# Kernel tuning notes

Hardware: AMD Instinct MI355X
Metric: run time of the kernel (lower is better)

## Reference

```python
import jax, jax.numpy as jnp
import numpy as np

N = 100_000      # number of sparse voxels / points
M = 1_000_000    # number of kernel-map (key,query) pairs
C_IN = 128
C_OUT = 128
H = 8            # num_heads
CH = C_OUT // H  # attn_channels = 16
KVOL = 27        # kernel_volume for kernel_size=3, dim=3
EPS_BN = 1e-5
EPS_NORM = 1e-12


def _bn(x, gamma, beta):
    # BatchNorm1d in training mode: batch statistics over point dim
    mu = jnp.mean(x, axis=0)
    var = jnp.var(x, axis=0)
    return (x - mu) * jax.lax.rsqrt(var + EPS_BN) * gamma + beta


def _l2norm(x):
    # F.normalize(p=2, dim=-1) with eps clamp
    n = jnp.sqrt(jnp.sum(x * x, axis=-1, keepdims=True))
    return x / jnp.maximum(n, EPS_NORM)


def setup_inputs() -> dict:
    key = jax.random.key(0)
    ks = jax.random.split(key, 14)
    inp = {
        "points": jax.random.normal(ks[0], (N, 3), jnp.float32),
        "feats": jax.random.normal(ks[1], (N, C_IN), jnp.float32),
        "k_idx": jax.random.randint(ks[2], (M,), 0, N),
        "q_idx": jax.random.randint(ks[3], (M,), 0, N),
        "kernel_idx": jax.random.randint(ks[4], (M,), 0, KVOL),
        # intra_pos_mlp params: Linear(3,3,no bias)-BN-ReLU-Linear(3,C_IN,no bias)-BN-ReLU-Linear(C_IN,C_IN)
        "w1": jax.random.normal(ks[5], (3, 3), jnp.float32) / np.float32(np.sqrt(3.0)),
        "g1": jnp.ones((3,), jnp.float32),
        "b1": jnp.zeros((3,), jnp.float32),
        "w2": jax.random.normal(ks[6], (3, C_IN), jnp.float32) / np.float32(np.sqrt(3.0)),
        "g2": jnp.ones((C_IN,), jnp.float32),
        "b2": jnp.zeros((C_IN,), jnp.float32),
        "w3": jax.random.normal(ks[7], (C_IN, C_IN), jnp.float32) / np.float32(np.sqrt(C_IN)),
        "b3": jnp.zeros((C_IN,), jnp.float32),
        # to_query / to_value (1x1 Minkowski conv == per-point linear) and to_out
        "wq": jax.random.normal(ks[8], (C_IN, C_OUT), jnp.float32) / np.float32(np.sqrt(C_IN)),
        "bq": jnp.zeros((C_OUT,), jnp.float32),
        "wv": jax.random.normal(ks[9], (C_IN, C_OUT), jnp.float32) / np.float32(np.sqrt(C_IN)),
        "bv": jnp.zeros((C_OUT,), jnp.float32),
        "wo": jax.random.normal(ks[10], (C_OUT, C_OUT), jnp.float32) / np.float32(np.sqrt(C_OUT)),
        "bo": jnp.zeros((C_OUT,), jnp.float32),
        # inter_pos_enc ~ N(0,1) per nn.init.normal_
        "pos_enc": jax.random.normal(ks[11], (KVOL, H, CH), jnp.float32),
    }
    return inp


def reference(points, feats, k_idx, q_idx, kernel_idx,
              w1, g1, b1, w2, g2, b2, w3, b3,
              wq, bq, wv, bv, wo, bo, pos_enc):
    # intra positional encoding MLP, added to features
    h = jax.nn.relu(_bn(points @ w1, g1, b1))
    h = jax.nn.relu(_bn(h @ w2, g2, b2))
    x = feats + (h @ w3 + b3)                       # [N, C_IN]
    # per-point query / value projections
    q = (x @ wq + bq).reshape(N, H, CH)             # [N, H, CH]
    v = (x @ wv + bv).reshape(N, H, CH)
    qn = _l2norm(q)
    pn = _l2norm(pos_enc)                           # [KVOL, H, CH]
    # DotProduct op: attn[m,h] = <norm_q[q_idx[m],h], norm_pos_enc[kernel_idx[m],h]>
    attn = jnp.einsum('mhc,mhc->mh', qn[q_idx], pn[kernel_idx])  # [M, H]
    # ScalarAttention op: out[q_idx[m],h,:] += attn[m,h] * v[k_idx[m],h,:]
    out = jnp.zeros((N, H, CH), feats.dtype).at[q_idx].add(attn[:, :, None] * v[k_idx])
    # to_out linear
    return out.reshape(N, C_OUT) @ wo + bo          # [N, C_OUT]
```

## Files before the change

### kernel.cpp

```cpp
#include <hip/hip_runtime.h>
#include <hip/hip_bf16.h>

#define CIN 128
#define NHEAD 8
#define CHD 16
#define KVOL 27
#define NBKT_MAX 512
#define CH 4096
#define NB1 64
#define NB2 256

constexpr float EPS_BN = 1e-5f;
constexpr float EPS_NORM = 1e-12f;

typedef __attribute__((ext_vector_type(8))) short short8;
typedef __attribute__((ext_vector_type(4))) float f32x4;

__device__ __forceinline__ float bflo(unsigned u) {
  return __uint_as_float(u << 16);
}
__device__ __forceinline__ float bfhi(unsigned u) {
  return __uint_as_float(u & 0xffff0000u);
}
__device__ __forceinline__ float bfus(unsigned short u) {
  return __uint_as_float((unsigned)u << 16);
}
__device__ __forceinline__ unsigned pk2bf(float lo, float hi) {
  __hip_bfloat16 a = __float2bfloat16(lo), b = __float2bfloat16(hi);
  return (unsigned)*(unsigned short*)&a | ((unsigned)*(unsigned short*)&b << 16);
}

__global__ __launch_bounds__(256) void k_bn1_stats(
    const float* __restrict__ points, const float* __restrict__ w1,
    float* __restrict__ partials1, int N) {
  __shared__ float red[4][6];
  float w[9];
#pragma unroll
  for (int i = 0; i < 9; ++i) w[i] = w1[i];
  float s[3] = {0.f, 0.f, 0.f}, ss[3] = {0.f, 0.f, 0.f};
  for (int n = blockIdx.x * blockDim.x + threadIdx.x; n < N;
       n += gridDim.x * blockDim.x) {
    float p0 = points[3 * n], p1 = points[3 * n + 1], p2 = points[3 * n + 2];
#pragma unroll
    for (int j = 0; j < 3; ++j) {
      float y = p0 * w[j] + p1 * w[3 + j] + p2 * w[6 + j];
      s[j] += y;
      ss[j] += y * y;
    }
  }
#pragma unroll
  for (int j = 0; j < 3; ++j) {
    for (int off = 32; off > 0; off >>= 1) {
      s[j] += __shfl_down(s[j], off);
      ss[j] += __shfl_down(ss[j], off);
    }
  }
  int t = threadIdx.x;
  if ((t & 63) == 0) {
    int wv = t >> 6;
#pragma unroll
    for (int j = 0; j < 3; ++j) {
      red[wv][j] = s[j];
      red[wv][3 + j] = ss[j];
    }
  }
  __syncthreads();
  if (t < 6) {
    float acc = red[0][t] + red[1][t] + red[2][t] + red[3][t];
    partials1[blockIdx.x * 8 + t] = acc;
  }
}

__global__ __launch_bounds__(256) void k_bn2_stats(
    const float* __restrict__ points, const float* __restrict__ w1,
    const float* __restrict__ g1, const float* __restrict__ b1,
    const float* __restrict__ w2, const float* __restrict__ partials1,
    float* __restrict__ partials2, int N) {
  __shared__ float pa[256][3];
  int t = threadIdx.x;
  float w[9];
#pragma unroll
  for (int i = 0; i < 9; ++i) w[i] = w1[i];
  float st[6] = {0.f, 0.f, 0.f, 0.f, 0.f, 0.f};
  for (int b = 0; b < NB1; ++b)
#pragma unroll
    for (int j = 0; j < 6; ++j) st[j] += partials1[b * 8 + j];
  float sc1[3], sh1[3];
#pragma unroll
  for (int j = 0; j < 3; ++j) {
    float m = st[j] / (float)N;
    float var = st[3 + j] / (float)N - m * m;
    float sc = rsqrtf(var + EPS_BN) * g1[j];
    sc1[j] = sc;
    sh1[j] = b1[j] - m * sc;
  }
  int c = t & 127, half = t >> 7;
  float wc0 = w2[c], wc1 = w2[CIN + c], wc2 = w2[2 * CIN + c];
  float s = 0.f, ss = 0.f;
  for (int base = blockIdx.x * 256; base < N; base += gridDim.x * 256) {
    int np = min(256, N - base);
    __syncthreads();
    if (t < np) {
      int n = base + t;
      float p0 = points[3 * n], p1 = points[3 * n + 1], p2 = points[3 * n + 2];
      float y0 = p0 * w[0] + p1 * w[3] + p2 * w[6];
      float y1 = p0 * w[1] + p1 * w[4] + p2 * w[7];
      float y2 = p0 * w[2] + p1 * w[5] + p2 * w[8];
      pa[t][0] = fmaxf(y0 * sc1[0] + sh1[0], 0.f);
      pa[t][1] = fmaxf(y1 * sc1[1] + sh1[1], 0.f);
      pa[t][2] = fmaxf(y2 * sc1[2] + sh1[2], 0.f);
    }
    __syncthreads();
    for (int p = half; p < np; p += 2) {
      float y = pa[p][0] * wc0 + pa[p][1] * wc1 + pa[p][2] * wc2;
      s += y;
      ss += y * y;
    }
  }
  __syncthreads();
  float* red = (float*)pa;
  red[t] = s;
  red[256 + t] = ss;
  __syncthreads();
  if (t < 128) {
    partials2[blockIdx.x * CIN + t] = red[t] + red[128 + t];
    partials2[NB2 * CIN + blockIdx.x * CIN + t] =
        red[256 + t] + red[256 + 128 + t];
  }
}

__global__ __launch_bounds__(256) void k_red2(const float* __restrict__ partials1,
                                              const float* __restrict__ partials2,
                                              float* __restrict__ stats1,
                                              float* __restrict__ stats2) {
  int t = threadIdx.x;
  if (t < 128) {
    float s = 0.f, ss = 0.f;
    for (int b = 0; b < NB2; ++b) {
      s += partials2[b * CIN + t];
      ss += partials2[NB2 * CIN + b * CIN + t];
    }
    stats2[t] = s;
    stats2[CIN + t] = ss;
  } else if (t < 134) {
    int j = t - 128;
    float s = 0.f;
    for (int b = 0; b < NB1; ++b) s += partials1[b * 8 + j];
    stats1[j] = s;
  }
}

__global__ void k_prep(const float* __restrict__ pos_enc,
                       const float* __restrict__ wq,
                       const float* __restrict__ wv,
                       const float* __restrict__ wo,
                       const float* __restrict__ w3,
                       __hip_bfloat16* __restrict__ pnb,
                       __hip_bfloat16* __restrict__ wqT,
                       __hip_bfloat16* __restrict__ wvT,
                       __hip_bfloat16* __restrict__ woT,
                       __hip_bfloat16* __restrict__ w3b) {
  int g = blockIdx.x * 256 + threadIdx.x;
  if (g < 256) {
    int kk = g >> 3, h = g & 7;
    if (kk < KVOL) {
      const float* src = pos_enc + (kk * NHEAD + h) * CHD;
      float vals[CHD];
      float s = 0.f;
#pragma unroll
      for (int i = 0; i < CHD; ++i) {
        vals[i] = src[i];
        s += vals[i] * vals[i];
      }
      float inv = 1.f / fmaxf(sqrtf(s), EPS_NORM);
#pragma unroll
      for (int i = 0; i < CHD; ++i)
        pnb[kk * CIN + h * CHD + i] = __float2bfloat16(vals[i] * inv);
    } else {
#pragma unroll
      for (int i = 0; i < CHD; ++i)
        pnb[kk * CIN + h * CHD + i] = __float2bfloat16(0.f);
    }
  }
  if (g < CIN * CIN) {
    int k = g >> 7, c = g & 127;
    int gt = c * CIN + k;
    wqT[gt] = __float2bfloat16(wq[g]);
    wvT[gt] = __float2bfloat16(wv[g]);
    woT[gt] = __float2bfloat16(wo[g]);
    w3b[g] = __float2bfloat16(w3[g]);
  }
}

__global__ __launch_bounds__(256) void k_prep2(
    const __hip_bfloat16* __restrict__ w3b,
    const __hip_bfloat16* __restrict__ wqT,
    const __hip_bfloat16* __restrict__ wvT, const float* __restrict__ wq,
    const float* __restrict__ wv, const float* __restrict__ b3,
    const float* __restrict__ bq, const float* __restrict__ bv,
    __hip_bfloat16* __restrict__ W3qT, __hip_bfloat16* __restrict__ W3vT,
    float* __restrict__ bqp, float* __restrict__ bvp) {
  int t = threadIdx.x;
  if (blockIdx.x == 4) {
    int c = t & 127;
    const float* wsel = (t < 128) ? wq : wv;
    float s = (t < 128) ? bq[c] : bv[c];
    for (int j = 0; j < CIN; ++j) s += b3[j] * wsel[j * CIN + c];
    if (t < 128)
      bqp[c] = s;
    else
      bvp[c] = s;
    return;
  }
  int n0 = blockIdx.x * 32;
  int w = t >> 6, l = t & 63;
  int lr = l & 15, lg = l >> 4;
  int colbase = w * 32;
  f32x4 cq[2][2], cv[2][2];
#pragma unroll
  for (int mt = 0; mt < 2; ++mt)
#pragma unroll
    for (int nt = 0; nt < 2; ++nt) {
      cq[mt][nt] = {0.f, 0.f, 0.f, 0.f};
      cv[mt][nt] = {0.f, 0.f, 0.f, 0.f};
    }
#pragma unroll
  for (int kk = 0; kk < 4; ++kk) {
    short8 aA[2], bQ[2], bV[2];
#pragma unroll
    for (int mt = 0; mt < 2; ++mt)
      aA[mt] = *(const short8*)(w3b + (size_t)(n0 + mt * 16 + lr) * CIN +
                                kk * 32 + lg * 8);
#pragma unroll
    for (int nt = 0; nt < 2; ++nt) {
      size_t off = (size_t)(colbase + nt * 16 + lr) * CIN + kk * 32 + lg * 8;
      bQ[nt] = *(const short8*)(wqT + off);
      bV[nt] = *(const short8*)(wvT + off);
    }
#pragma unroll
    for (int mt = 0; mt < 2; ++mt)
#pragma unroll
      for (int nt = 0; nt < 2; ++nt) {
        cq[mt][nt] = __builtin_amdgcn_mfma_f32_16x16x32_bf16(aA[mt], bQ[nt],
                                                             cq[mt][nt], 0, 0, 0);
        cv[mt][nt] = __builtin_amdgcn_mfma_f32_16x16x32_bf16(aA[mt], bV[nt],
                                                             cv[mt][nt], 0, 0, 0);
      }
  }
#pragma unroll
  for (int mt = 0; mt < 2; ++mt)
#pragma unroll
    for (int nt = 0; nt < 2; ++nt)
#pragma unroll
      for (int r = 0; r < 4; ++r) {
        int k = n0 + mt * 16 + lg * 4 + r;
        int c = colbase + nt * 16 + lr;
        W3qT[(size_t)c * CIN + k] = __float2bfloat16(cq[mt][nt][r]);
        W3vT[(size_t)c * CIN + k] = __float2bfloat16(cv[mt][nt][r]);
      }
}

__global__ __launch_bounds__(256) void k_chist(const int* __restrict__ q_idx,
                                               int* __restrict__ ccnt, int M) {
  __shared__ int lh[NBKT_MAX];
  int t = threadIdx.x;
  for (int b = t; b < NBKT_MAX; b += 256) lh[b] = 0;
  __syncthreads();
  for (int i = blockIdx.x * 256 + t; i < M; i += gridDim.x * 256)
    atomicAdd(&lh[q_idx[i] >> 8], 1);
  __syncthreads();
  for (int b = t; b < NBKT_MAX; b += 256) {
    int c = lh[b];
    if (c > 0) atomicAdd(&ccnt[b], c);
  }
}

__global__ __launch_bounds__(256) void k_cscan(const int* __restrict__ ccnt,
                                               int* __restrict__ sbase,
                                               int* __restrict__ bcur) {
  __shared__ int wsum[4];
  int t = threadIdx.x;
  int s0 = ccnt[2 * t], s1 = ccnt[2 * t + 1];
  int s = s0 + s1;
  int l = t & 63, w = t >> 6;
  int ss = s;
  for (int off = 1; off < 64; off <<= 1) {
    int v = __shfl_up(ss, off);
    if (l >= off) ss += v;
  }
  if (l == 63) wsum[w] = ss;
  __syncthreads();
  int wb = 0;
#pragma unroll
  for (int i = 0; i < 4; ++i)
    if (i < w) wb += wsum[i];
  int ex = wb + ss - s;
  sbase[2 * t] = ex;
  sbase[2 * t + 1] = ex + s0;
  bcur[2 * t] = ex;
  bcur[2 * t + 1] = ex + s0;
  if (t == 255) sbase[NBKT_MAX] = wb + ss;
}

__global__ __launch_bounds__(256) void k_bucket1(
    const int* __restrict__ q_idx, const int* __restrict__ k_idx,
    const int* __restrict__ kernel_idx, int* __restrict__ bcur,
    unsigned* __restrict__ stg, int M) {
  __shared__ int lhist[NBKT_MAX];
  __shared__ int loffs[NBKT_MAX];
  __shared__ int lcur[NBKT_MAX];
  __shared__ int wsum[4];
  __shared__ unsigned buf[CH];
  int t = threadIdx.x;
  int base = blockIdx.x * CH;
  for (int b = t; b < NBKT_MAX; b += 256) lhist[b] = 0;
  __syncthreads();

  int qv[16];
#pragma unroll
  for (int j = 0; j < 16; ++j) {
    int i = base + t + j * 256;
    int q = (i < M) ? q_idx[i] : -1;
    qv[j] = q;
    if (q >= 0) atomicAdd(&lhist[q >> 8], 1);
  }
  __syncthreads();

  {
    int s0 = lhist[2 * t], s1 = lhist[2 * t + 1];
    int s = s0 + s1;
    int l = t & 63, w = t >> 6;
    int ss = s;
    for (int off = 1; off < 64; off <<= 1) {
      int v = __shfl_up(ss, off);
      if (l >= off) ss += v;
    }
    if (l == 63) wsum[w] = ss;
    __syncthreads();
    int wb = 0;
#pragma unroll
    for (int i = 0; i < 4; ++i)
      if (i < w) wb += wsum[i];
    int ex = wb + ss - s;
    loffs[2 * t] = ex;
    loffs[2 * t + 1] = ex + s0;
    lcur[2 * t] = ex;
    lcur[2 * t + 1] = ex + s0;
  }
  __syncthreads();

#pragma unroll
  for (int j = 0; j < 16; ++j) {
    int q = qv[j];
    if (q >= 0) {
      int i = base + t + j * 256;
      unsigned e = (unsigned)k_idx[i] | ((unsigned)kernel_idx[i] << 17) |
                   ((unsigned)(q & 255) << 22);
      int d = atomicAdd(&lcur[q >> 8], 1);
      buf[d] = e;
    }
  }
  __syncthreads();

  for (int b = t; b < NBKT_MAX; b += 256) {
    int cntb = lhist[b];
    if (cntb > 0) {
      int g = atomicAdd(&bcur[b], cntb);
      int lo = loffs[b];
      for (int j = 0; j < cntb; ++j) stg[g + j] = buf[lo + j];
    }
  }
}

__global__ __launch_bounds__(256) void k_bucket2a(
    const unsigned* __restrict__ stg, const int* __restrict__ sbase,
    int* __restrict__ cnt, int N) {
  __shared__ int lh[256];
  int b = blockIdx.x;
  int t = threadIdx.x;
  lh[t] = 0;
  __syncthreads();
  int start = sbase[b];
  int bcnt = sbase[b + 1] - start;
  for (int i = t; i < bcnt; i += 256) atomicAdd(&lh[stg[start + i] >> 22], 1);
  __syncthreads();
  int q = (b << 8) + t;
  if (q < N) cnt[q] = lh[t];
}

__global__ __launch_bounds__(256) void k_scan1(const int* __restrict__ cnt,
                                               int* __restrict__ poffs,
                                               int* __restrict__ bsum, int N) {
  __shared__ int ws_[4];
  int t = threadIdx.x;
  int l = t & 63, w = t >> 6;
  int base = blockIdx.x * 1024 + t * 4;
  int pc[4];
  int s = 0;
#pragma unroll
  for (int j = 0; j < 4; ++j) {
    int c = (base + j < N) ? cnt[base + j] : 0;
    pc[j] = (c + 7) & ~7;
// ... 31 lines not shown
    int v = __shfl_up(s, off);
    if (l >= off) s += v;
  }
  if (l == 63) ws_[w] = s;
  __syncthreads();
  int wbase = 0;
#pragma unroll
  for (int i = 0; i < 4; ++i)
    if (i < w) wbase += ws_[i];
  if (t < NB) bbase[t] = wbase + s - own;
  if (t == 255) *poffsN = wbase + s;
}

__global__ __launch_bounds__(256) void k_scan3(const int* __restrict__ cnt,
                                               int* __restrict__ poffs,
                                               const int* __restrict__ bbase,
                                               unsigned* __restrict__ recs,
                                               int N) {
  int t = threadIdx.x;
  int base = blockIdx.x * 1024 + t * 4;
  int bb = bbase[blockIdx.x];
#pragma unroll
  for (int j = 0; j < 4; ++j) {
    int i = base + j;
    if (i >= N) break;
    int o = poffs[i] + bb;
    poffs[i] = o;
    int c = cnt[i];
    int pcend = o + ((c + 7) & ~7);
    for (int p = o + c; p < pcend; ++p) recs[p] = 27u << 17;
  }
}

__global__ __launch_bounds__(256) void k_bucket2b(
    const unsigned* __restrict__ stg, const int* __restrict__ sbase,
    const int* __restrict__ poffs, unsigned* __restrict__ recs, int N) {
  __shared__ int qcur[256];
  int b = blockIdx.x;
  int t = threadIdx.x;
  int qbase = b << 8;
  int q = qbase + t;
  qcur[t] = (q < N) ? poffs[q] : 0;
  __syncthreads();
  int start = sbase[b];
  int bcnt = sbase[b + 1] - start;
  for (int i = t; i < bcnt; i += 256) {
    unsigned e = stg[start + i];
    int ql = e >> 22;
    unsigned rec = e & 0x3FFFFFu;
    int pos = atomicAdd(&qcur[ql], 1);
    recs[pos] = rec;
  }
}

__global__ __launch_bounds__(256) void k_qv(
    const float* __restrict__ points, const float* __restrict__ feats,
    const float* __restrict__ w1, const float* __restrict__ g1,
    const float* __restrict__ b1, const float* __restrict__ w2,
    const float* __restrict__ g2, const float* __restrict__ b2,
    const __hip_bfloat16* __restrict__ wqT,
    const __hip_bfloat16* __restrict__ wvT,
    const __hip_bfloat16* __restrict__ W3qT,
    const __hip_bfloat16* __restrict__ W3vT, const float* __restrict__ bqp,
    const float* __restrict__ bvp, const float* __restrict__ stats1,
    const float* __restrict__ stats2, __hip_bfloat16* __restrict__ qnout,
    __hip_bfloat16* __restrict__ vout, int N) {
  __shared__ float h0s[32][3];
  __shared__ __hip_bfloat16 h1s[32][136];
  __shared__ __hip_bfloat16 fs[32][136];

  int t = threadIdx.x;
  int n0 = blockIdx.x * 32;

  int frow = t >> 3, fpart = t & 7;
  int fn = n0 + frow;
  float4 f0 = {0.f, 0.f, 0.f, 0.f}, f1 = f0, f2 = f0, f3 = f0;
  if (fn < N) {
    const float4* src = (const float4*)(feats + (size_t)fn * CIN + fpart * 16);
    f0 = src[0];
    f1 = src[1];
    f2 = src[2];
    f3 = src[3];
  }

  if (t < 32) {
    int n = n0 + t;
    float p0 = 0.f, p1 = 0.f, p2 = 0.f;
    if (n < N) {
      p0 = points[3 * n];
      p1 = points[3 * n + 1];
      p2 = points[3 * n + 2];
    }
#pragma unroll
    for (int j = 0; j < 3; ++j) {
      float m = stats1[j] / (float)N;
      float var = stats1[3 + j] / (float)N - m * m;
      float sc = rsqrtf(var + EPS_BN) * g1[j];
      float sh = b1[j] - m * sc;
      float y = p0 * w1[j] + p1 * w1[3 + j] + p2 * w1[6 + j];
      h0s[t][j] = fmaxf(y * sc + sh, 0.f);
    }
  }

  {
    unsigned u[8];
// ... 91 lines not shown
        s += __shfl_xor(s, 4);
        s += __shfl_xor(s, 8);
        float inv = 1.f / fmaxf(sqrtf(s), EPS_NORM);
        int row = mt * 16 + lg * 4 + r;
        int col = colbase + nt * 16 + lr;
        fs[row][col] = __float2bfloat16(q * inv);
        h1s[row][col] = __float2bfloat16(av[mt][nt][r]);
      }
  __syncthreads();

  {
    int row = t >> 3, part = t & 7;
    int n = n0 + row;
    if (n < N) {
      const char* srcq = (const char*)&fs[row][0] + part * 32;
      char* dstq = (char*)qnout + (size_t)n * 256 + part * 32;
      *(uint4*)dstq = *(const uint4*)srcq;
      *(uint4*)(dstq + 16) = *(const uint4*)(srcq + 16);
      const char* srcv = (const char*)&h1s[row][0] + part * 32;
      char* dstv = (char*)vout + (size_t)n * 256 + part * 32;
      *(uint4*)dstv = *(const uint4*)srcv;
      *(uint4*)(dstv + 16) = *(const uint4*)(srcv + 16);
    }
  }
}

__global__ __launch_bounds__(512) void k_gather_out(
    const unsigned* __restrict__ recs, const int* __restrict__ poffs,
    const __hip_bfloat16* __restrict__ qn, const __hip_bfloat16* __restrict__ v,
    const __hip_bfloat16* __restrict__ pnb,
    const __hip_bfloat16* __restrict__ woT, const float* __restrict__ bo,
    float* __restrict__ out, int N) {
  __shared__ __hip_bfloat16 accs[32][136];
  __shared__ unsigned short dotlds[32][256];
  int t = threadIdx.x;
  int w = t >> 6, l = t & 63;
  int h = l >> 3;
  int n0 = blockIdx.x * 32;
  const char* vbase = (const char*)v + 4 * l;

  {
    int row = t >> 4, part = t & 15;
    int n = n0 + row;
    uint4 val = {0u, 0u, 0u, 0u};
    if (n < N)
      val = *(const uint4*)((const char*)qn + (size_t)n * 256 + part * 16);
    *(uint4*)((char*)&accs[row][0] + part * 16) = val;
  }
  __syncthreads();

  {
    int lr = l & 15, lg = l >> 4;
    int rg = w & 1;
    const short8 zero8 = {0, 0, 0, 0, 0, 0, 0, 0};
#pragma unroll
    for (int hh = 0; hh < 2; ++hh) {
      int hx = (w >> 1) * 2 + hh;
      short8 aA = zero8, bB0 = zero8, bB1 = zero8;
      if (lg < 2) {
        aA = *(const short8*)((const char*)&accs[rg * 16 + lr][0] +
                              (hx * CHD + lg * 8) * 2);
        bB0 = *(const short8*)(pnb + lr * CIN + hx * CHD + lg * 8);
        bB1 = *(const short8*)(pnb + (16 + lr) * CIN + hx * CHD + lg * 8);
      }
      f32x4 c0 = {0.f, 0.f, 0.f, 0.f}, c1 = {0.f, 0.f, 0.f, 0.f};
      c0 = __builtin_amdgcn_mfma_f32_16x16x32_bf16(aA, bB0, c0, 0, 0, 0);
      c1 = __builtin_amdgcn_mfma_f32_16x16x32_bf16(aA, bB1, c1, 0, 0, 0);
#pragma unroll
      for (int r = 0; r < 4; ++r) {
        int row = rg * 16 + lg * 4 + r;
        __hip_bfloat16 b0 = __float2bfloat16(c0[r]);
        __hip_bfloat16 b1 = __float2bfloat16(c1[r]);
        dotlds[row][lr * 8 + hx] = *(unsigned short*)&b0;
        dotlds[row][(16 + lr) * 8 + hx] = *(unsigned short*)&b1;
      }
    }
  }
  __syncthreads();

#pragma unroll 1
  for (int j = 0; j < 4; ++j) {
    int nl = w * 4 + j;
    int n = n0 + nl;
    float ax = 0.f, ay = 0.f;
    if (n < N) {
      const unsigned short* dptr = &dotlds[nl][0];
      int beg = poffs[n], end = poffs[n + 1];
      for (int idx = beg; idx < end; idx += 8) {
        unsigned r0 = recs[idx + 0], r1 = recs[idx + 1], r2 = recs[idx + 2],
                 r3 = recs[idx + 3], r4 = recs[idx + 4], r5 = recs[idx + 5],
                 r6 = recs[idx + 6], r7 = recs[idx + 7];
        unsigned v0 = *(const unsigned*)(vbase + (size_t)(r0 & 0x1FFFF) * 256);
        unsigned v1 = *(const unsigned*)(vbase + (size_t)(r1 & 0x1FFFF) * 256);
        unsigned v2 = *(const unsigned*)(vbase + (size_t)(r2 & 0x1FFFF) * 256);
        unsigned v3 = *(const unsigned*)(vbase + (size_t)(r3 & 0x1FFFF) * 256);
        unsigned v4 = *(const unsigned*)(vbase + (size_t)(r4 & 0x1FFFF) * 256);
        unsigned v5 = *(const unsigned*)(vbase + (size_t)(r5 & 0x1FFFF) * 256);
        unsigned v6 = *(const unsigned*)(vbase + (size_t)(r6 & 0x1FFFF) * 256);
        unsigned v7 = *(const unsigned*)(vbase + (size_t)(r7 & 0x1FFFF) * 256);
        float a0 = bfus(dptr[(r0 >> 17) * 8 + h]);
        float a1 = bfus(dptr[(r1 >> 17) * 8 + h]);
        float a2 = bfus(dptr[(r2 >> 17) * 8 + h]);
        float a3 = bfus(dptr[(r3 >> 17) * 8 + h]);
        float a4 = bfus(dptr[(r4 >> 17) * 8 + h]);
        float a5 = bfus(dptr[(r5 >> 17) * 8 + h]);
        float a6 = bfus(dptr[(r6 >> 17) * 8 + h]);
        float a7 = bfus(dptr[(r7 >> 17) * 8 + h]);
        ax += a0 * bflo(v0);
        ay += a0 * bfhi(v0);
        ax += a1 * bflo(v1);
        ay += a1 * bfhi(v1);
        ax += a2 * bflo(v2);
        ay += a2 * bfhi(v2);
        ax += a3 * bflo(v3);
        ay += a3 * bfhi(v3);
        ax += a4 * bflo(v4);
        ay += a4 * bfhi(v4);
        ax += a5 * bflo(v5);
        ay += a5 * bfhi(v5);
        ax += a6 * bflo(v6);
        ay += a6 * bfhi(v6);
        ax += a7 * bflo(v7);
        ay += a7 * bfhi(v7);
      }
    }
    __hip_bfloat16 bx = __float2bfloat16(ax), by = __float2bfloat16(ay);
    unsigned pk = (unsigned)*(unsigned short*)&bx |
                  ((unsigned)*(unsigned short*)&by << 16);
    ((unsigned*)((char*)accs + nl * 272))[l] = pk;
  }
  __syncthreads();

  int lr = l & 15, lg = l >> 4;
  int colb = w * 16;
  float bc = bo[colb + lr];
  f32x4 acc0 = {bc, bc, bc, bc}, acc1 = {bc, bc, bc, bc};
#pragma unroll
  for (int kk = 0; kk < 4; ++kk) {
    short8 aA0 = *(const short8*)((const char*)accs + lr * 272 +
                                  (kk * 32 + lg * 8) * 2);
// ... 12 lines not shown
    if (nr1 < N) out[(size_t)nr1 * CIN + colb + lr] = acc1[r];
  }
}

extern "C" void kernel_launch(void* const* d_in, const int* in_sizes, int n_in,
                              void* d_out, int out_size, void* d_ws,
                              size_t ws_size, hipStream_t stream) {
  const float* points = (const float*)d_in[0];
  const float* feats = (const float*)d_in[1];
  const int* k_idx = (const int*)d_in[2];
  const int* q_idx = (const int*)d_in[3];
  const int* kernel_idx = (const int*)d_in[4];
  const float* w1 = (const float*)d_in[5];
  const float* g1 = (const float*)d_in[6];
  const float* b1 = (const float*)d_in[7];
  const float* w2 = (const float*)d_in[8];
  const float* g2 = (const float*)d_in[9];
  const float* b2 = (const float*)d_in[10];
  const float* w3 = (const float*)d_in[11];
  const float* b3 = (const float*)d_in[12];
  const float* wq = (const float*)d_in[13];
  const float* bq = (const float*)d_in[14];
  const float* wv = (const float*)d_in[15];
  const float* bv = (const float*)d_in[16];
  const float* wo = (const float*)d_in[17];
  const float* bo = (const float*)d_in[18];
  const float* pos_enc = (const float*)d_in[19];

  int N = in_sizes[0] / 3;
  int M = in_sizes[2];
  int NB = (N + 1023) / 1024;
  int NBKT = (N + 255) >> 8;
  int Np = (N + 4) & ~3;

  float* ws = (float*)d_ws;
  float* stats1 = ws;
  float* stats2 = ws + 8;
  __hip_bfloat16* pnb = (__hip_bfloat16*)(ws + 264);
  float* bqp = ws + 2312;
  float* bvp = ws + 2440;
  int* cnt = (int*)(ws + 4096);
  int* poffs = cnt + Np;
  int* bsum = poffs + Np;
  int* bbase = bsum + 512;
  int* bcur = bbase + 512;
  int* ccnt = bcur + 512;
  int* sbase = ccnt + 512;
  unsigned* recs = (unsigned*)(sbase + 520);
  size_t recn = ((size_t)M + 8 * (size_t)N + 7) & ~(size_t)7;
  unsigned* stg = recs + recn;
  __hip_bfloat16* qnb = (__hip_bfloat16*)(stg + M);
  __hip_bfloat16* vb = qnb + (size_t)N * CIN;
  __hip_bfloat16* wqT = vb + (size_t)N * CIN;
  __hip_bfloat16* wvT = wqT + CIN * CIN;
  __hip_bfloat16* woT = wvT + CIN * CIN;
  __hip_bfloat16* W3qT = woT + CIN * CIN;
  __hip_bfloat16* W3vT = W3qT + CIN * CIN;
  __hip_bfloat16* w3b = W3vT + CIN * CIN;
  float* partials1 = (float*)(w3b + CIN * CIN);
  float* partials2 = partials1 + NB1 * 8;
  float* outf = (float*)d_out;

  hipMemsetAsync(ccnt, 0, NBKT_MAX * sizeof(int), stream);

  k_bn1_stats<<<NB1, 256, 0, stream>>>(points, w1, partials1, N);
  k_prep<<<64, 256, 0, stream>>>(pos_enc, wq, wv, wo, w3, pnb, wqT, wvT, woT,
                                 w3b);
  k_bn2_stats<<<NB2, 256, 0, stream>>>(points, w1, g1, b1, w2, partials1,
                                       partials2, N);
  k_prep2<<<5, 256, 0, stream>>>(w3b, wqT, wvT, wq, wv, b3, bq, bv, W3qT, W3vT,
                                 bqp, bvp);
  k_red2<<<1, 256, 0, stream>>>(partials1, partials2, stats1, stats2);
  k_chist<<<256, 256, 0, stream>>>(q_idx, ccnt, M);
  k_cscan<<<1, 256, 0, stream>>>(ccnt, sbase, bcur);
  k_bucket1<<<(M + CH - 1) / CH, 256, 0, stream>>>(q_idx, k_idx, kernel_idx,
                                                   bcur, stg, M);
  k_bucket2a<<<NBKT, 256, 0, stream>>>(stg, sbase, cnt, N);
  k_scan1<<<NB, 256, 0, stream>>>(cnt, poffs, bsum, N);
  k_scan2<<<1, 256, 0, stream>>>(bsum, bbase, NB, poffs + N);
  k_scan3<<<NB, 256, 0, stream>>>(cnt, poffs, bbase, recs, N);
  k_bucket2b<<<NBKT, 256, 0, stream>>>(stg, sbase, poffs, recs, N);
  k_qv<<<(N + 31) / 32, 256, 0, stream>>>(points, feats, w1, g1, b1, w2, g2, b2,
                                          wqT, wvT, W3qT, W3vT, bqp, bvp,
                                          stats1, stats2, qnb, vb, N);
  k_gather_out<<<(N + 31) / 32, 512, 0, stream>>>(recs, poffs, qnb, vb, pnb,
                                                  woT, bo, outf, N);
}
```

Baseline: 248.4 us.

## Merge independent preprocessing kernels into block-partitioned fused launches

Independent setup kernels (BN stats, weight prep, histogram, bucket scan, bucket scatter, Q/V projection) are merged into fewer launches, with each block picking its role from its block index. This cuts launch count and the idle gaps between small serialized kernels. Separately, the attention dot products kept in LDS switch from bf16 to fp32 in a smaller padded array, which drops the conversion on read. The cost is larger shared-memory footprints per fused kernel, possible occupancy changes, and load imbalance between blocks doing different roles.

```diff
diff --git a/kernel.cpp b/kernel.cpp
--- a/kernel.cpp
+++ b/kernel.cpp
@@ -22,352 +22,341 @@
 __device__ __forceinline__ float bfhi(unsigned u) {
   return __uint_as_float(u & 0xffff0000u);
 }
-__device__ __forceinline__ float bfus(unsigned short u) {
-  return __uint_as_float((unsigned)u << 16);
-}
 __device__ __forceinline__ unsigned pk2bf(float lo, float hi) {
   __hip_bfloat16 a = __float2bfloat16(lo), b = __float2bfloat16(hi);
   return (unsigned)*(unsigned short*)&a | ((unsigned)*(unsigned short*)&b << 16);
 }
 
-__global__ __launch_bounds__(256) void k_bn1_stats(
+__global__ __launch_bounds__(256) void k_fuseA(
     const float* __restrict__ points, const float* __restrict__ w1,
-    float* __restrict__ partials1, int N) {
-  __shared__ float red[4][6];
-  float w[9];
-#pragma unroll
-  for (int i = 0; i < 9; ++i) w[i] = w1[i];
-  float s[3] = {0.f, 0.f, 0.f}, ss[3] = {0.f, 0.f, 0.f};
-  for (int n = blockIdx.x * blockDim.x + threadIdx.x; n < N;
-       n += gridDim.x * blockDim.x) {
-    float p0 = points[3 * n], p1 = points[3 * n + 1], p2 = points[3 * n + 2];
+    float* __restrict__ partials1, const float* __restrict__ pos_enc,
+    const float* __restrict__ wq, const float* __restrict__ wv,
+    const float* __restrict__ wo, const float* __restrict__ w3,
+    __hip_bfloat16* __restrict__ pnb, __hip_bfloat16* __restrict__ wqT,
+    __hip_bfloat16* __restrict__ wvT, __hip_bfloat16* __restrict__ woT,
+    __hip_bfloat16* __restrict__ w3b, const int* __restrict__ q_idx,
+    int* __restrict__ ccnt, int N, int M) {
+  __shared__ __align__(16) char smem[2048];
+  int bid = blockIdx.x;
+  int t = threadIdx.x;
+  if (bid < 64) {
+    float(*red)[6] = (float(*)[6])smem;
+    float w[9];
+#pragma unroll
+    for (int i = 0; i < 9; ++i) w[i] = w1[i];
+    float s[3] = {0.f, 0.f, 0.f}, ss[3] = {0.f, 0.f, 0.f};
+    for (int n = bid * 256 + t; n < N; n += 64 * 256) {
+      float p0 = points[3 * n], p1 = points[3 * n + 1], p2 = points[3 * n + 2];
+#pragma unroll
+      for (int j = 0; j < 3; ++j) {
+        float y = p0 * w[j] + p1 * w[3 + j] + p2 * w[6 + j];
+        s[j] += y;
+        ss[j] += y * y;
+      }
+    }
 #pragma unroll
     for (int j = 0; j < 3; ++j) {
-      float y = p0 * w[j] + p1 * w[3 + j] + p2 * w[6 + j];
-      s[j] += y;
-      ss[j] += y * y;
-    }
-  }
-#pragma unroll
-  for (int j = 0; j < 3; ++j) {
-    for (int off = 32; off > 0; off >>= 1) {
-      s[j] += __shfl_down(s[j], off);
-      ss[j] += __shfl_down(ss[j], off);
-    }
-  }
-  int t = threadIdx.x;
-  if ((t & 63) == 0) {
-    int wv = t >> 6;
-#pragma unroll
-    for (int j = 0; j < 3; ++j) {
-      red[wv][j] = s[j];
-      red[wv][3 + j] = ss[j];
-    }
-  }
-  __syncthreads();
-  if (t < 6) {
-    float acc = red[0][t] + red[1][t] + red[2][t] + red[3][t];
-    partials1[blockIdx.x * 8 + t] = acc;
-  }
-}
-
-__global__ __launch_bounds__(256) void k_bn2_stats(
+      for (int off = 32; off > 0; off >>= 1) {
+        s[j] += __shfl_down(s[j], off);
+        ss[j] += __shfl_down(ss[j], off);
+      }
+    }
+    if ((t & 63) == 0) {
+      int wv_ = t >> 6;
+#pragma unroll
+      for (int j = 0; j < 3; ++j) {
+        red[wv_][j] = s[j];
+        red[wv_][3 + j] = ss[j];
+      }
+    }
+    __syncthreads();
+    if (t < 6) {
+      float acc = red[0][t] + red[1][t] + red[2][t] + red[3][t];
+      partials1[bid * 8 + t] = acc;
+    }
+  } else if (bid < 128) {
+    int g = (bid - 64) * 256 + t;
+    if (g < 256) {
+      int kk = g >> 3, h = g & 7;
+      if (kk < KVOL) {
+        const float* src = pos_enc + (kk * NHEAD + h) * CHD;
+        float vals[CHD];
+        float s = 0.f;
+#pragma unroll
+        for (int i = 0; i < CHD; ++i) {
+          vals[i] = src[i];
+          s += vals[i] * vals[i];
+        }
+        float inv = 1.f / fmaxf(sqrtf(s), EPS_NORM);
+#pragma unroll
+        for (int i = 0; i < CHD; ++i)
+          pnb[kk * CIN + h * CHD + i] = __float2bfloat16(vals[i] * inv);
+      } else {
+#pragma unroll
+        for (int i = 0; i < CHD; ++i)
+          pnb[kk * CIN + h * CHD + i] = __float2bfloat16(0.f);
+      }
+    }
+    if (g < CIN * CIN) {
+      int k = g >> 7, c = g & 127;
+      int gt = c * CIN + k;
+      wqT[gt] = __float2bfloat16(wq[g]);
+      wvT[gt] = __float2bfloat16(wv[g]);
+      woT[gt] = __float2bfloat16(wo[g]);
+      w3b[g] = __float2bfloat16(w3[g]);
+    }
+  } else {
+    int* lh = (int*)smem;
+    for (int b = t; b < NBKT_MAX; b += 256) lh[b] = 0;
+    __syncthreads();
+    for (int i = (bid - 128) * 256 + t; i < M; i += 256 * 256)
+      atomicAdd(&lh[q_idx[i] >> 8], 1);
+    __syncthreads();
+    for (int b = t; b < NBKT_MAX; b += 256) {
+      int c = lh[b];
+      if (c > 0) atomicAdd(&ccnt[b], c);
+    }
+  }
+}
+
+__global__ __launch_bounds__(256) void k_fuseB(
     const float* __restrict__ points, const float* __restrict__ w1,
     const float* __restrict__ g1, const float* __restrict__ b1,
     const float* __restrict__ w2, const float* __restrict__ partials1,
-    float* __restrict__ partials2, int N) {
-  __shared__ float pa[256][3];
+    float* __restrict__ partials2, const int* __restrict__ ccnt,
+    int* __restrict__ sbase, int* __restrict__ bcur, int N) {
+  __shared__ __align__(16) char smem[3072];
   int t = threadIdx.x;
-  float w[9];
-#pragma unroll
-  for (int i = 0; i < 9; ++i) w[i] = w1[i];
-  float st[6] = {0.f, 0.f, 0.f, 0.f, 0.f, 0.f};
-  for (int b = 0; b < NB1; ++b)
-#pragma unroll
-    for (int j = 0; j < 6; ++j) st[j] += partials1[b * 8 + j];
-  float sc1[3], sh1[3];
-#pragma unroll
-  for (int j = 0; j < 3; ++j) {
-    float m = st[j] / (float)N;
-    float var = st[3 + j] / (float)N - m * m;
-    float sc = rsqrtf(var + EPS_BN) * g1[j];
-    sc1[j] = sc;
-    sh1[j] = b1[j] - m * sc;
-  }
-  int c = t & 127, half = t >> 7;
-  float wc0 = w2[c], wc1 = w2[CIN + c], wc2 = w2[2 * CIN + c];
-  float s = 0.f, ss = 0.f;
-  for (int base = blockIdx.x * 256; base < N; base += gridDim.x * 256) {
-    int np = min(256, N - base);
-    __syncthreads();
-    if (t < np) {
-      int n = base + t;
-      float p0 = points[3 * n], p1 = points[3 * n + 1], p2 = points[3 * n + 2];
-      float y0 = p0 * w[0] + p1 * w[3] + p2 * w[6];
-      float y1 = p0 * w[1] + p1 * w[4] + p2 * w[7];
-      float y2 = p0 * w[2] + p1 * w[5] + p2 * w[8];
-      pa[t][0] = fmaxf(y0 * sc1[0] + sh1[0], 0.f);
-      pa[t][1] = fmaxf(y1 * sc1[1] + sh1[1], 0.f);
-      pa[t][2] = fmaxf(y2 * sc1[2] + sh1[2], 0.f);
-    }
-    __syncthreads();
-    for (int p = half; p < np; p += 2) {
-      float y = pa[p][0] * wc0 + pa[p][1] * wc1 + pa[p][2] * wc2;
-      s += y;
-      ss += y * y;
-    }
-  }
-  __syncthreads();
-  float* red = (float*)pa;
-  red[t] = s;
-  red[256 + t] = ss;
-  __syncthreads();
-  if (t < 128) {
-    partials2[blockIdx.x * CIN + t] = red[t] + red[128 + t];
-    partials2[NB2 * CIN + blockIdx.x * CIN + t] =
-        red[256 + t] + red[256 + 128 + t];
-  }
-}
-
-__global__ __launch_bounds__(256) void k_red2(const float* __restrict__ partials1,
-                                              const float* __restrict__ partials2,
-                                              float* __restrict__ stats1,
-                                              float* __restrict__ stats2) {
-  int t = threadIdx.x;
-  if (t < 128) {
+  if (blockIdx.x < NB2) {
+    float(*pa)[3] = (float(*)[3])smem;
+    float w[9];
+#pragma unroll
+    for (int i = 0; i < 9; ++i) w[i] = w1[i];
+    float st[6] = {0.f, 0.f, 0.f, 0.f, 0.f, 0.f};
+    for (int b = 0; b < NB1; ++b)
+#pragma unroll
+      for (int j = 0; j < 6; ++j) st[j] += partials1[b * 8 + j];
+    float sc1[3], sh1[3];
+#pragma unroll
+    for (int j = 0; j < 3; ++j) {
+      float m = st[j] / (float)N;
+      float var = st[3 + j] / (float)N - m * m;
+      float sc = rsqrtf(var + EPS_BN) * g1[j];
+      sc1[j] = sc;
+      sh1[j] = b1[j] - m * sc;
+    }
+    int c = t & 127, half = t >> 7;
+    float wc0 = w2[c], wc1 = w2[CIN + c], wc2 = w2[2 * CIN + c];
     float s = 0.f, ss = 0.f;
-    for (int b = 0; b < NB2; ++b) {
-      s += partials2[b * CIN + t];
-      ss += partials2[NB2 * CIN + b * CIN + t];
-    }
-    stats2[t] = s;
-    stats2[CIN + t] = ss;
-  } else if (t < 134) {
-    int j = t - 128;
-    float s = 0.f;
-    for (int b = 0; b < NB1; ++b) s += partials1[b * 8 + j];
-    stats1[j] = s;
-  }
-}
-
-__global__ void k_prep(const float* __restrict__ pos_enc,
-                       const float* __restrict__ wq,
-                       const float* __restrict__ wv,
-                       const float* __restrict__ wo,
-                       const float* __restrict__ w3,
-                       __hip_bfloat16* __restrict__ pnb,
-                       __hip_bfloat16* __restrict__ wqT,
-                       __hip_bfloat16* __restrict__ wvT,
-                       __hip_bfloat16* __restrict__ woT,
-                       __hip_bfloat16* __restrict__ w3b) {
-  int g = blockIdx.x * 256 + threadIdx.x;
-  if (g < 256) {
-    int kk = g >> 3, h = g & 7;
-    if (kk < KVOL) {
-      const float* src = pos_enc + (kk * NHEAD + h) * CHD;
-      float vals[CHD];
-      float s = 0.f;
-#pragma unroll
-      for (int i = 0; i < CHD; ++i) {
-        vals[i] = src[i];
-        s += vals[i] * vals[i];
-      }
-      float inv = 1.f / fmaxf(sqrtf(s), EPS_NORM);
-#pragma unroll
-      for (int i = 0; i < CHD; ++i)
-        pnb[kk * CIN + h * CHD + i] = __float2bfloat16(vals[i] * inv);
-    } else {
-#pragma unroll
-      for (int i = 0; i < CHD; ++i)
-        pnb[kk * CIN + h * CHD + i] = __float2bfloat16(0.f);
-    }
-  }
-  if (g < CIN * CIN) {
-    int k = g >> 7, c = g & 127;
-    int gt = c * CIN + k;
-    wqT[gt] = __float2bfloat16(wq[g]);
-    wvT[gt] = __float2bfloat16(wv[g]);
-    woT[gt] = __float2bfloat16(wo[g]);
-    w3b[g] = __float2bfloat16(w3[g]);
-  }
-}
-
-__global__ __launch_bounds__(256) void k_prep2(
+    for (int base = blockIdx.x * 256; base < N; base += NB2 * 256) {
+      int np = min(256, N - base);
+      __syncthreads();
+      if (t < np) {
+        int n = base + t;
+        float p0 = points[3 * n], p1 = points[3 * n + 1],
+              p2 = points[3 * n + 2];
+        float y0 = p0 * w[0] + p1 * w[3] + p2 * w[6];
+        float y1 = p0 * w[1] + p1 * w[4] + p2 * w[7];
+        float y2 = p0 * w[2] + p1 * w[5] + p2 * w[8];
+        pa[t][0] = fmaxf(y0 * sc1[0] + sh1[0], 0.f);
+        pa[t][1] = fmaxf(y1 * sc1[1] + sh1[1], 0.f);
+        pa[t][2] = fmaxf(y2 * sc1[2] + sh1[2], 0.f);
+      }
+      __syncthreads();
+      for (int p = half; p < np; p += 2) {
+        float y = pa[p][0] * wc0 + pa[p][1] * wc1 + pa[p][2] * wc2;
+        s += y;
+        ss += y * y;
+      }
+    }
+    __syncthreads();
+    float* red = (float*)pa;
+    red[t] = s;
+    red[256 + t] = ss;
+    __syncthreads();
+    if (t < 128) {
+      partials2[blockIdx.x * CIN + t] = red[t] + red[128 + t];
+      partials2[NB2 * CIN + blockIdx.x * CIN + t] =
+          red[256 + t] + red[256 + 128 + t];
+    }
+  } else {
+    int* wsum = (int*)smem;
+    int s0 = ccnt[2 * t], s1 = ccnt[2 * t + 1];
+    int s = s0 + s1;
+    int l = t & 63, w = t >> 6;
+    int ss = s;
+    for (int off = 1; off < 64; off <<= 1) {
+      int v = __shfl_up(ss, off);
+      if (l >= off) ss += v;
+    }
+    if (l == 63) wsum[w] = ss;
+    __syncthreads();
+    int wb = 0;
+#pragma unroll
+    for (int i = 0; i < 4; ++i)
+      if (i < w) wb += wsum[i];
+    int ex = wb + ss - s;
+    sbase[2 * t] = ex;
+    sbase[2 * t + 1] = ex + s0;
+    bcur[2 * t] = ex;
+    bcur[2 * t + 1] = ex + s0;
+    if (t == 255) sbase[NBKT_MAX] = wb + ss;
+  }
+}
+
+__global__ __launch_bounds__(256) void k_fuseC(
+    const float* __restrict__ partials1, const float* __restrict__ partials2,
+    float* __restrict__ stats1, float* __restrict__ stats2,
     const __hip_bfloat16* __restrict__ w3b,
     const __hip_bfloat16* __restrict__ wqT,
     const __hip_bfloat16* __restrict__ wvT, const float* __restrict__ wq,
     const float* __restrict__ wv, const float* __restrict__ b3,
     const float* __restrict__ bq, const float* __restrict__ bv,
     __hip_bfloat16* __restrict__ W3qT, __hip_bfloat16* __restrict__ W3vT,
-    float* __restrict__ bqp, float* __restrict__ bvp) {
-  int t = threadIdx.x;
-  if (blockIdx.x == 4) {
-    int c = t & 127;
-    const float* wsel = (t < 128) ? wq : wv;
-    float s = (t < 128) ? bq[c] : bv[c];
-    for (int j = 0; j < CIN; ++j) s += b3[j] * wsel[j * CIN + c];
-    if (t < 128)
-      bqp[c] = s;
-    else
-      bvp[c] = s;
-    return;
-  }
-  int n0 = blockIdx.x * 32;
-  int w = t >> 6, l = t & 63;
-  int lr = l & 15, lg = l >> 4;
-  int colbase = w * 32;
-  f32x4 cq[2][2], cv[2][2];
-#pragma unroll
-  for (int mt = 0; mt < 2; ++mt)
-#pragma unroll
-    for (int nt = 0; nt < 2; ++nt) {
-      cq[mt][nt] = {0.f, 0.f, 0.f, 0.f};
-      cv[mt][nt] = {0.f, 0.f, 0.f, 0.f};
-    }
-#pragma unroll
-  for (int kk = 0; kk < 4; ++kk) {
-    short8 aA[2], bQ[2], bV[2];
-#pragma unroll
-    for (int mt = 0; mt < 2; ++mt)
-      aA[mt] = *(const short8*)(w3b + (size_t)(n0 + mt * 16 + lr) * CIN +
-                                kk * 32 + lg * 8);
-#pragma unroll
-    for (int nt = 0; nt < 2; ++nt) {
-      size_t off = (size_t)(colbase + nt * 16 + lr) * CIN + kk * 32 + lg * 8;
-      bQ[nt] = *(const short8*)(wqT + off);
-      bV[nt] = *(const short8*)(wvT + off);
-    }
-#pragma unroll
-    for (int mt = 0; mt < 2; ++mt)
-#pragma unroll
-      for (int nt = 0; nt < 2; ++nt) {
-        cq[mt][nt] = __builtin_amdgcn_mfma_f32_16x16x32_bf16(aA[mt], bQ[nt],
-                                                             cq[mt][nt], 0, 0, 0);
-        cv[mt][nt] = __builtin_amdgcn_mfma_f32_16x16x32_bf16(aA[mt], bV[nt],
-                                                             cv[mt][nt], 0, 0, 0);
-      }
-  }
-#pragma unroll
-  for (int mt = 0; mt < 2; ++mt)
-#pragma unroll
-    for (int nt = 0; nt < 2; ++nt)
-#pragma unroll
-      for (int r = 0; r < 4; ++r) {
-        int k = n0 + mt * 16 + lg * 4 + r;
-        int c = colbase + nt * 16 + lr;
-        W3qT[(size_t)c * CIN + k] = __float2bfloat16(cq[mt][nt][r]);
-        W3vT[(size_t)c * CIN + k] = __float2bfloat16(cv[mt][nt][r]);
-      }
-}
-
-__global__ __launch_bounds__(256) void k_chist(const int* __restrict__ q_idx,
-                                               int* __restrict__ ccnt, int M) {
-  __shared__ int lh[NBKT_MAX];
-  int t = threadIdx.x;
-  for (int b = t; b < NBKT_MAX; b += 256) lh[b] = 0;
-  __syncthreads();
-  for (int i = blockIdx.x * 256 + t; i < M; i += gridDim.x * 256)
-    atomicAdd(&lh[q_idx[i] >> 8], 1);
-  __syncthreads();
-  for (int b = t; b < NBKT_MAX; b += 256) {
-    int c = lh[b];
-    if (c > 0) atomicAdd(&ccnt[b], c);
-  }
-}
-
-__global__ __launch_bounds__(256) void k_cscan(const int* __restrict__ ccnt,
-                                               int* __restrict__ sbase,
-                                               int* __restrict__ bcur) {
-  __shared__ int wsum[4];
-  int t = threadIdx.x;
-  int s0 = ccnt[2 * t], s1 = ccnt[2 * t + 1];
-  int s = s0 + s1;
-  int l = t & 63, w = t >> 6;
-  int ss = s;
-  for (int off = 1; off < 64; off <<= 1) {
-    int v = __shfl_up(ss, off);
-    if (l >= off) ss += v;
-  }
-  if (l == 63) wsum[w] = ss;
-  __syncthreads();
-  int wb = 0;
-#pragma unroll
-  for (int i = 0; i < 4; ++i)
-    if (i < w) wb += wsum[i];
-  int ex = wb + ss - s;
-  sbase[2 * t] = ex;
-  sbase[2 * t + 1] = ex + s0;
-  bcur[2 * t] = ex;
-  bcur[2 * t + 1] = ex + s0;
-  if (t == 255) sbase[NBKT_MAX] = wb + ss;
-}
-
-__global__ __launch_bounds__(256) void k_bucket1(
+    float* __restrict__ bqp, float* __restrict__ bvp,
     const int* __restrict__ q_idx, const int* __restrict__ k_idx,
     const int* __restrict__ kernel_idx, int* __restrict__ bcur,
     unsigned* __restrict__ stg, int M) {
-  __shared__ int lhist[NBKT_MAX];
-  __shared__ int loffs[NBKT_MAX];
-  __shared__ int lcur[NBKT_MAX];
-  __shared__ int wsum[4];
-  __shared__ unsigned buf[CH];
+  __shared__ __align__(16) char smem[22544];
+  int bid = blockIdx.x;
   int t = threadIdx.x;
-  int base = blockIdx.x * CH;
-  for (int b = t; b < NBKT_MAX; b += 256) lhist[b] = 0;
-  __syncthreads();
-
-  int qv[16];
-#pragma unroll
-  for (int j = 0; j < 16; ++j) {
-    int i = base + t + j * 256;
-    int q = (i < M) ? q_idx[i] : -1;
-    qv[j] = q;
-    if (q >= 0) atomicAdd(&lhist[q >> 8], 1);
-  }
-  __syncthreads();
-
-  {
-    int s0 = lhist[2 * t], s1 = lhist[2 * t + 1];
-    int s = s0 + s1;
-    int l = t & 63, w = t >> 6;
-    int ss = s;
-    for (int off = 1; off < 64; off <<= 1) {
-      int v = __shfl_up(ss, off);
-      if (l >= off) ss += v;
-    }
-    if (l == 63) wsum[w] = ss;
-    __syncthreads();
-    int wb = 0;
-#pragma unroll
-    for (int i = 0; i < 4; ++i)
-      if (i < w) wb += wsum[i];
-    int ex = wb + ss - s;
-    loffs[2 * t] = ex;
-    loffs[2 * t + 1] = ex + s0;
-    lcur[2 * t] = ex;
-    lcur[2 * t + 1] = ex + s0;
-  }
-  __syncthreads();
-
-#pragma unroll
-  for (int j = 0; j < 16; ++j) {
-    int q = qv[j];
-    if (q >= 0) {
+  if (bid == 0) {
+    if (t < 128) {
+      float s = 0.f, ss = 0.f;
+      for (int b = 0; b < NB2; ++b) {
+        s += partials2[b * CIN + t];
+        ss += partials2[NB2 * CIN + b * CIN + t];
+      }
+      stats2[t] = s;
+      stats2[CIN + t] = ss;
+    } else if (t < 134) {
+      int j = t - 128;
+      float s = 0.f;
+      for (int b = 0; b < NB1; ++b) s += partials1[b * 8 + j];
+      stats1[j] = s;
+    }
+  } else if (bid < 6) {
+    int pb = bid - 1;
+    if (pb == 4) {
+      int c = t & 127;
+      const float* wsel = (t < 128) ? wq : wv;
+      float s = (t < 128) ? bq[c] : bv[c];
+      for (int j = 0; j < CIN; ++j) s += b3[j] * wsel[j * CIN + c];
+      if (t < 128)
+        bqp[c] = s;
+      else
+        bvp[c] = s;
+      return;
+    }
+    int n0 = pb * 32;
+    int w = t >> 6, l = t & 63;
+    int lr = l & 15, lg = l >> 4;
+    int colbase = w * 32;
+    f32x4 cq[2][2], cv[2][2];
+#pragma unroll
+    for (int mt = 0; mt < 2; ++mt)
+#pragma unroll
+      for (int nt = 0; nt < 2; ++nt) {
+        cq[mt][nt] = {0.f, 0.f, 0.f, 0.f};
+        cv[mt][nt] = {0.f, 0.f, 0.f, 0.f};
+      }
+#pragma unroll
+    for (int kk = 0; kk < 4; ++kk) {
+      short8 aA[2], bQ[2], bV[2];
+#pragma unroll
+      for (int mt = 0; mt < 2; ++mt)
+        aA[mt] = *(const short8*)(w3b + (size_t)(n0 + mt * 16 + lr) * CIN +
+                                  kk * 32 + lg * 8);
+#pragma unroll
+      for (int nt = 0; nt < 2; ++nt) {
+        size_t off = (size_t)(colbase + nt * 16 + lr) * CIN + kk * 32 + lg * 8;
+        bQ[nt] = *(const short8*)(wqT + off);
+        bV[nt] = *(const short8*)(wvT + off);
+      }
+#pragma unroll
+      for (int mt = 0; mt < 2; ++mt)
+#pragma unroll
+        for (int nt = 0; nt < 2; ++nt) {
+          cq[mt][nt] = __builtin_amdgcn_mfma_f32_16x16x32_bf16(
+              aA[mt], bQ[nt], cq[mt][nt], 0, 0, 0);
+          cv[mt][nt] = __builtin_amdgcn_mfma_f32_16x16x32_bf16(
+              aA[mt], bV[nt], cv[mt][nt], 0, 0, 0);
+        }
+    }
+#pragma unroll
+    for (int mt = 0; mt < 2; ++mt)
+#pragma unroll
+      for (int nt = 0; nt < 2; ++nt)
+#pragma unroll
+        for (int r = 0; r < 4; ++r) {
+          int k = n0 + mt * 16 + lg * 4 + r;
+          int c = colbase + nt * 16 + lr;
+          W3qT[(size_t)c * CIN + k] = __float2bfloat16(cq[mt][nt][r]);
+          W3vT[(size_t)c * CIN + k] = __float2bfloat16(cv[mt][nt][r]);
+        }
+  } else {
+    int* lhist = (int*)smem;
+    int* loffs = (int*)(smem + 2048);
+    int* lcur = (int*)(smem + 4096);
+    int* wsum = (int*)(smem + 6144);
+    unsigned* buf = (unsigned*)(smem + 6160);
+    int base = (bid - 6) * CH;
+    for (int b = t; b < NBKT_MAX; b += 256) lhist[b] = 0;
+    __syncthreads();
+
+    int qv_[16];
+#pragma unroll
+    for (int j = 0; j < 16; ++j) {
       int i = base + t + j * 256;
-      unsigned e = (unsigned)k_idx[i] | ((unsigned)kernel_idx[i] << 17) |
-                   ((unsigned)(q & 255) << 22);
-      int d = atomicAdd(&lcur[q >> 8], 1);
-      buf[d] = e;
-    }
-  }
-  __syncthreads();
-
-  for (int b = t; b < NBKT_MAX; b += 256) {
-    int cntb = lhist[b];
-    if (cntb > 0) {
-      int g = atomicAdd(&bcur[b], cntb);
-      int lo = loffs[b];
-      for (int j = 0; j < cntb; ++j) stg[g + j] = buf[lo + j];
+      int q = (i < M) ? q_idx[i] : -1;
+      qv_[j] = q;
+      if (q >= 0) atomicAdd(&lhist[q >> 8], 1);
+    }
+    __syncthreads();
+
+    {
+      int s0 = lhist[2 * t], s1 = lhist[2 * t + 1];
+      int s = s0 + s1;
+      int l = t & 63, w = t >> 6;
+      int ss = s;
+      for (int off = 1; off < 64; off <<= 1) {
+        int v = __shfl_up(ss, off);
+        if (l >= off) ss += v;
+      }
+      if (l == 63) wsum[w] = ss;
+      __syncthreads();
+      int wb = 0;
+#pragma unroll
+      for (int i = 0; i < 4; ++i)
+        if (i < w) wb += wsum[i];
+      int ex = wb + ss - s;
+      loffs[2 * t] = ex;
+      loffs[2 * t + 1] = ex + s0;
+      lcur[2 * t] = ex;
+      lcur[2 * t + 1] = ex + s0;
+    }
+    __syncthreads();
+
+#pragma unroll
+    for (int j = 0; j < 16; ++j) {
+      int q = qv_[j];
+      if (q >= 0) {
+        int i = base + t + j * 256;
+        unsigned e = (unsigned)k_idx[i] | ((unsigned)kernel_idx[i] << 17) |
+                     ((unsigned)(q & 255) << 22);
+        int d = atomicAdd(&lcur[q >> 8], 1);
+        buf[d] = e;
+      }
+    }
+    __syncthreads();
+
+    for (int b = t; b < NBKT_MAX; b += 256) {
+      int cntb = lhist[b];
+      if (cntb > 0) {
+        int g = atomicAdd(&bcur[b], cntb);
+        int lo = loffs[b];
+        for (int j = 0; j < cntb; ++j) stg[g + j] = buf[lo + j];
+      }
     }
   }
 }
@@ -465,28 +454,9 @@
   }
 }
 
-__global__ __launch_bounds__(256) void k_bucket2b(
+__global__ __launch_bounds__(256) void k_qv_b2b(
     const unsigned* __restrict__ stg, const int* __restrict__ sbase,
-    const int* __restrict__ poffs, unsigned* __restrict__ recs, int N) {
-  __shared__ int qcur[256];
-  int b = blockIdx.x;
-  int t = threadIdx.x;
-  int qbase = b << 8;
-  int q = qbase + t;
-  qcur[t] = (q < N) ? poffs[q] : 0;
-  __syncthreads();
-  int start = sbase[b];
-  int bcnt = sbase[b + 1] - start;
-  for (int i = t; i < bcnt; i += 256) {
-    unsigned e = stg[start + i];
-    int ql = e >> 22;
-    unsigned rec = e & 0x3FFFFFu;
-    int pos = atomicAdd(&qcur[ql], 1);
-    recs[pos] = rec;
-  }
-}
-
-__global__ __launch_bounds__(256) void k_qv(
+    const int* __restrict__ poffs, unsigned* __restrict__ recs, int NBKT,
     const float* __restrict__ points, const float* __restrict__ feats,
     const float* __restrict__ w1, const float* __restrict__ g1,
     const float* __restrict__ b1, const float* __restrict__ w2,
@@ -498,12 +468,31 @@
     const float* __restrict__ bvp, const float* __restrict__ stats1,
     const float* __restrict__ stats2, __hip_bfloat16* __restrict__ qnout,
     __hip_bfloat16* __restrict__ vout, int N) {
-  __shared__ float h0s[32][3];
-  __shared__ __hip_bfloat16 h1s[32][136];
-  __shared__ __hip_bfloat16 fs[32][136];
-
+  __shared__ __align__(16) char smem[17792];
   int t = threadIdx.x;
-  int n0 = blockIdx.x * 32;
+  if ((int)blockIdx.x < NBKT) {
+    int* qcur = (int*)smem;
+    int b = blockIdx.x;
+    int qbase = b << 8;
+    int q = qbase + t;
+    qcur[t] = (q < N) ? poffs[q] : 0;
+    __syncthreads();
+    int start = sbase[b];
+    int bcnt = sbase[b + 1] - start;
+    for (int i = t; i < bcnt; i += 256) {
+      unsigned e = stg[start + i];
+      int ql = e >> 22;
+      unsigned rec = e & 0x3FFFFFu;
+      int pos = atomicAdd(&qcur[ql], 1);
+      recs[pos] = rec;
+    }
+    return;
+  }
+  float(*h0s)[3] = (float(*)[3])smem;
+  __hip_bfloat16(*h1s)[136] = (__hip_bfloat16(*)[136])(smem + 384);
+  __hip_bfloat16(*fs)[136] = (__hip_bfloat16(*)[136])(smem + 9088);
+
+  int n0 = ((int)blockIdx.x - NBKT) * 32;
 
   int frow = t >> 3, fpart = t & 7;
   int fn = n0 + frow;
@@ -661,7 +650,7 @@
     const __hip_bfloat16* __restrict__ woT, const float* __restrict__ bo,
     float* __restrict__ out, int N) {
   __shared__ __hip_bfloat16 accs[32][136];
-  __shared__ unsigned short dotlds[32][256];
+  __shared__ float dotlds[32][224];
   int t = threadIdx.x;
   int w = t >> 6, l = t & 63;
   int h = l >> 3;
@@ -698,10 +687,8 @@
 #pragma unroll
       for (int r = 0; r < 4; ++r) {
         int row = rg * 16 + lg * 4 + r;
-        __hip_bfloat16 b0 = __float2bfloat16(c0[r]);
-        __hip_bfloat16 b1 = __float2bfloat16(c1[r]);
-        dotlds[row][lr * 8 + hx] = *(unsigned short*)&b0;
-        dotlds[row][(16 + lr) * 8 + hx] = *(unsigned short*)&b1;
+        dotlds[row][lr * 8 + hx] = c0[r];
+        if (lr < 12) dotlds[row][(16 + lr) * 8 + hx] = c1[r];
       }
     }
   }
@@ -713,7 +700,7 @@
     int n = n0 + nl;
     float ax = 0.f, ay = 0.f;
     if (n < N) {
-      const unsigned short* dptr = &dotlds[nl][0];
+      const float* dptr = &dotlds[nl][0];
       int beg = poffs[n], end = poffs[n + 1];
       for (int idx = beg; idx < end; idx += 8) {
         unsigned r0 = recs[idx + 0], r1 = recs[idx + 1], r2 = recs[idx + 2],
@@ -727,14 +714,14 @@
         unsigned v5 = *(const unsigned*)(vbase + (size_t)(r5 & 0x1FFFF) * 256);
         unsigned v6 = *(const unsigned*)(vbase + (size_t)(r6 & 0x1FFFF) * 256);
         unsigned v7 = *(const unsigned*)(vbase + (size_t)(r7 & 0x1FFFF) * 256);
-        float a0 = bfus(dptr[(r0 >> 17) * 8 + h]);
-        float a1 = bfus(dptr[(r1 >> 17) * 8 + h]);
-        float a2 = bfus(dptr[(r2 >> 17) * 8 + h]);
-        float a3 = bfus(dptr[(r3 >> 17) * 8 + h]);
-        float a4 = bfus(dptr[(r4 >> 17) * 8 + h]);
-        float a5 = bfus(dptr[(r5 >> 17) * 8 + h]);
-        float a6 = bfus(dptr[(r6 >> 17) * 8 + h]);
-        float a7 = bfus(dptr[(r7 >> 17) * 8 + h]);
+        float a0 = dptr[(r0 >> 17) * 8 + h];
+        float a1 = dptr[(r1 >> 17) * 8 + h];
+        float a2 = dptr[(r2 >> 17) * 8 + h];
+        float a3 = dptr[(r3 >> 17) * 8 + h];
+        float a4 = dptr[(r4 >> 17) * 8 + h];
+        float a5 = dptr[(r5 >> 17) * 8 + h];
+        float a6 = dptr[(r6 >> 17) * 8 + h];
+        float a7 = dptr[(r7 >> 17) * 8 + h];
         ax += a0 * bflo(v0);
         ay += a0 * bfhi(v0);
         ax += a1 * bflo(v1);
@@ -813,6 +800,7 @@
   int NB = (N + 1023) / 1024;
   int NBKT = (N + 255) >> 8;
   int Np = (N + 4) & ~3;
+  int NB1C = (M + CH - 1) / CH;
 
   float* ws = (float*)d_ws;
   float* stats1 = ws;
@@ -844,26 +832,22 @@
 
   hipMemsetAsync(ccnt, 0, NBKT_MAX * sizeof(int), stream);
 
-  k_bn1_stats<<<NB1, 256, 0, stream>>>(points, w1, partials1, N);
-  k_prep<<<64, 256, 0, stream>>>(pos_enc, wq, wv, wo, w3, pnb, wqT, wvT, woT,
-                                 w3b);
-  k_bn2_stats<<<NB2, 256, 0, stream>>>(points, w1, g1, b1, w2, partials1,
-                                       partials2, N);
-  k_prep2<<<5, 256, 0, stream>>>(w3b, wqT, wvT, wq, wv, b3, bq, bv, W3qT, W3vT,
-                                 bqp, bvp);
-  k_red2<<<1, 256, 0, stream>>>(partials1, partials2, stats1, stats2);
-  k_chist<<<256, 256, 0, stream>>>(q_idx, ccnt, M);
-  k_cscan<<<1, 256, 0, stream>>>(ccnt, sbase, bcur);
-  k_bucket1<<<(M + CH - 1) / CH, 256, 0, stream>>>(q_idx, k_idx, kernel_idx,
-                                                   bcur, stg, M);
+  k_fuseA<<<384, 256, 0, stream>>>(points, w1, partials1, pos_enc, wq, wv, wo,
+                                   w3, pnb, wqT, wvT, woT, w3b, q_idx, ccnt, N,
+                                   M);
+  k_fuseB<<<NB2 + 1, 256, 0, stream>>>(points, w1, g1, b1, w2, partials1,
+                                       partials2, ccnt, sbase, bcur, N);
+  k_fuseC<<<6 + NB1C, 256, 0, stream>>>(partials1, partials2, stats1, stats2,
+                                        w3b, wqT, wvT, wq, wv, b3, bq, bv, W3qT,
+                                        W3vT, bqp, bvp, q_idx, k_idx,
+                                        kernel_idx, bcur, stg, M);
   k_bucket2a<<<NBKT, 256, 0, stream>>>(stg, sbase, cnt, N);
   k_scan1<<<NB, 256, 0, stream>>>(cnt, poffs, bsum, N);
   k_scan2<<<1, 256, 0, stream>>>(bsum, bbase, NB, poffs + N);
   k_scan3<<<NB, 256, 0, stream>>>(cnt, poffs, bbase, recs, N);
-  k_bucket2b<<<NBKT, 256, 0, stream>>>(stg, sbase, poffs, recs, N);
-  k_qv<<<(N + 31) / 32, 256, 0, stream>>>(points, feats, w1, g1, b1, w2, g2, b2,
-                                          wqT, wvT, W3qT, W3vT, bqp, bvp,
-                                          stats1, stats2, qnb, vb, N);
+  k_qv_b2b<<<NBKT + (N + 31) / 32, 256, 0, stream>>>(
+      stg, sbase, poffs, recs, NBKT, points, feats, w1, g1, b1, w2, g2, b2, wqT,
+      wvT, W3qT, W3vT, bqp, bvp, stats1, stats2, qnb, vb, N);
   k_gather_out<<<(N + 31) / 32, 512, 0, stream>>>(recs, poffs, qnb, vb, pnb,
                                                   woT, bo, outf, N);
 }
```

After: 219.7 us. -11.5%, faster.
